# Performance work log

Hardware: AMD Instinct MI355X
Metric: run time of the kernel (lower is better)

## Reference

```python
import jax, jax.numpy as jnp
import numpy as np

T, B, H, C = 4096, 32, 512, 32000

def setup_inputs() -> dict:
    key = jax.random.key(0)
    k1, k2, k3, k4, k5 = jax.random.split(key, 5)
    decoder_output = jax.random.normal(k1, (T, B, H), dtype=jnp.float32)
    align_w = jax.random.normal(k2, (H,), dtype=jnp.float32) * (1.0 / np.sqrt(H))
    align_b = jax.random.normal(k3, (), dtype=jnp.float32) * 0.01
    out_w = jax.random.normal(k4, (C, H), dtype=jnp.float32) * (1.0 / np.sqrt(H))
    out_b = jax.random.normal(k5, (C,), dtype=jnp.float32) * 0.01
    return {"decoder_output": decoder_output, "align_w": align_w,
            "align_b": align_b, "out_w": out_w, "out_b": out_b}

def reference(decoder_output, align_w, align_b, out_w, out_b):
    # e[b,t] = tanh(align(decoder_output[t,b]))  -- vectorized over (t,b)
    e = jnp.tanh(jnp.einsum('tbh,h->bt', decoder_output, align_w) + align_b)  # [B,T]
    alpha = jax.nn.softmax(e, axis=-1)                                        # [B,T]
    context = jnp.einsum('bt,tbh->bh', alpha, decoder_output)                 # [B,H]
    return context @ out_w.T + out_b                                          # [B,C]
```

## Files before the change

### kernel.cpp

```cpp
#include <hip/hip_runtime.h>
#include <hip/hip_bf16.h>
#include <math.h>

#define TT 4096
#define BB 32
#define HH 512
#define CC 32000
#define NCHUNK 64
#define TPC 64
#define HQ 4
#define OSLICE (BB*CC)
#define OW_PAD 36

#define WS_CTX    0
#define WS_LPART  16384
#define WS_BIG    18432

__device__ __forceinline__ float dot4(const float4 a, const float4 b) {
  return fmaf(a.w, b.w, fmaf(a.z, b.z, fmaf(a.y, b.y, fmaf(a.x, b.x, 0.f))));
}

__global__ __launch_bounds__(256) void k1_partials(
    const float* __restrict__ dec, const float* __restrict__ aw,
    const float* __restrict__ abp,
    float* __restrict__ ctx_part, float* __restrict__ l_part)
{
  const int chunk = blockIdx.x;
  const int b     = blockIdx.y;
  const int tid   = threadIdx.x;
  const int wv = tid >> 6, ln = tid & 63;
  const float ab = abp[0];
  const float4 aw0 = *(const float4*)(aw + ln*4);
  const float4 aw1 = *(const float4*)(aw + 256 + ln*4);

  const size_t rowstep = (size_t)BB*HH;
  const float* base = dec + ((size_t)(chunk*TPC + wv*16)*BB + b)*HH + (size_t)ln*4;

  float4 c0 = make_float4(0.f,0.f,0.f,0.f), c1 = make_float4(0.f,0.f,0.f,0.f);
  float l = 0.f;

  for (int it = 0; it < 16; it += 2) {
    const float* p0 = base + (size_t)it*rowstep;
    const float* p1 = base + (size_t)(it+1)*rowstep;
    const float4 xa0 = *(const float4*)(p0);
    const float4 xa1 = *(const float4*)(p0 + 256);
    const float4 xb0 = *(const float4*)(p1);
    const float4 xb1 = *(const float4*)(p1 + 256);
    float da = dot4(xa0, aw0) + dot4(xa1, aw1);
    float db = dot4(xb0, aw0) + dot4(xb1, aw1);
    #pragma unroll
    for (int off = 32; off > 0; off >>= 1) {
      da += __shfl_xor(da, off);
      db += __shfl_xor(db, off);
    }
    const float exa = __expf(2.f*(da + ab));
    const float exb = __expf(2.f*(db + ab));
    const float tha = 1.f - 2.f*__builtin_amdgcn_rcpf(exa + 1.f);
    const float thb = 1.f - 2.f*__builtin_amdgcn_rcpf(exb + 1.f);
    const float wa = __expf(tha);
    const float wb = __expf(thb);
    l += wa + wb;
    c0.x = fmaf(wa, xa0.x, fmaf(wb, xb0.x, c0.x));
    c0.y = fmaf(wa, xa0.y, fmaf(wb, xb0.y, c0.y));
    c0.z = fmaf(wa, xa0.z, fmaf(wb, xb0.z, c0.z));
    c0.w = fmaf(wa, xa0.w, fmaf(wb, xb0.w, c0.w));
    c1.x = fmaf(wa, xa1.x, fmaf(wb, xb1.x, c1.x));
    c1.y = fmaf(wa, xa1.y, fmaf(wb, xb1.y, c1.y));
    c1.z = fmaf(wa, xa1.z, fmaf(wb, xb1.z, c1.z));
    c1.w = fmaf(wa, xa1.w, fmaf(wb, xb1.w, c1.w));
  }

  __shared__ float s_ctx[4][HH];
  __shared__ float s_l[4];
  *(float4*)&s_ctx[wv][ln*4]       = c0;
  *(float4*)&s_ctx[wv][256 + ln*4] = c1;
  if (ln == 0) s_l[wv] = l;
  __syncthreads();
  if (tid < 128) {
    const int h = tid * 4;
    float4 a = make_float4(0.f,0.f,0.f,0.f);
    #pragma unroll
    for (int w2 = 0; w2 < 4; ++w2) {
      const float4 v = *(const float4*)&s_ctx[w2][h];
      a.x += v.x; a.y += v.y; a.z += v.z; a.w += v.w;
    }
    const size_t pp = (size_t)b*NCHUNK + chunk;
    *(float4*)(ctx_part + pp*HH + h) = a;
    if (tid == 0) l_part[pp] = s_l[0] + s_l[1] + s_l[2] + s_l[3];
  }
}

__global__ __launch_bounds__(128) void k2_combine(
    const float* __restrict__ ctx_part, const float* __restrict__ l_part,
    float* __restrict__ ctx)
{
  const int b = blockIdx.x;
  const int h = threadIdx.x * 4;
  float L = 0.f;
  for (int p = 0; p < NCHUNK; ++p) L += l_part[b*NCHUNK + p];
  float4 a = make_float4(0.f,0.f,0.f,0.f);
  for (int p = 0; p < NCHUNK; ++p) {
    const float4 v = *(const float4*)(ctx_part + ((size_t)b*NCHUNK + p)*HH + h);
    a.x += v.x; a.y += v.y; a.z += v.z; a.w += v.w;
  }
  const float inv = 1.f / L;
  *(float4*)(ctx + b*HH + h) = make_float4(a.x*inv, a.y*inv, a.z*inv, a.w*inv);
}

__global__ __launch_bounds__(256) void k3_matmul(
    const float* __restrict__ ctx, const float* __restrict__ ow,
    float* __restrict__ out_part)
{
  __shared__ float s_ow[256*OW_PAD];
  __shared__ float s_cx[32*128];
  const int tid = threadIdx.x;
  const int ci = tid & 63, wv = tid >> 6;
  const int hq = blockIdx.x, cblk = blockIdx.y;
  const int h0 = hq * 128;
  const int crow0 = cblk * 256;

  #pragma unroll
  for (int rep = 0; rep < 4; ++rep) {
    const int j = rep*1024 + tid*4;
    const int b = j >> 7, hh = j & 127;
    *(float4*)&s_cx[j] = *(const float4*)(ctx + (size_t)b*HH + h0 + hh);
  }

  float acc[4][8];
  #pragma unroll
  for (int g = 0; g < 4; ++g)
    #pragma unroll
    for (int bi = 0; bi < 8; ++bi) acc[g][bi] = 0.f;

  for (int ch = 0; ch < 4; ++ch) {
    if (ch) __syncthreads();
    #pragma unroll
    for (int rep = 0; rep < 8; ++rep) {
      const int j = rep*256 + tid;
      const int r = j >> 3, hp = j & 7;
      *(float4*)&s_ow[r*OW_PAD + hp*4] =
          *(const float4*)(ow + (size_t)(crow0 + r)*HH + h0 + ch*32 + hp*4);
    }
    __syncthreads();
    #pragma unroll
    for (int s = 0; s < 8; ++s) {
      float4 w4[4];
      #pragma unroll
      for (int g = 0; g < 4; ++g)
        w4[g] = *(const float4*)&s_ow[(g*64 + ci)*OW_PAD + s*4];
      #pragma unroll
      for (int bi = 0; bi < 8; ++bi) {
        const float4 c4 = *(const float4*)&s_cx[(wv*8 + bi)*128 + ch*32 + s*4];
        #pragma unroll
        for (int g = 0; g < 4; ++g) {
          acc[g][bi] = fmaf(w4[g].w, c4.w, fmaf(w4[g].z, c4.z,
                       fmaf(w4[g].y, c4.y, fmaf(w4[g].x, c4.x, acc[g][bi]))));
        }
      }
    }
  }

  float* op = out_part + (size_t)hq*OSLICE;
  #pragma unroll
  for (int bi = 0; bi < 8; ++bi) {
    #pragma unroll
    for (int g = 0; g < 4; ++g)
      op[(size_t)(wv*8 + bi)*CC + crow0 + g*64 + ci] = acc[g][bi];
  }
}

__global__ __launch_bounds__(256) void k4_final(
    const float* __restrict__ out_part, const float* __restrict__ ob,
    float* __restrict__ out)
{
  const size_t i = ((size_t)blockIdx.x * 256 + threadIdx.x) * 4;
  float4 r = *(const float4*)(out_part + i);
  #pragma unroll
  for (int q = 1; q < HQ; ++q) {
    const float4 p = *(const float4*)(out_part + (size_t)q*OSLICE + i);
    r.x += p.x; r.y += p.y; r.z += p.z; r.w += p.w;
  }
  const int cIdx = (int)(i % CC);
  const float4 b4 = *(const float4*)(ob + cIdx);
  *(float4*)(out + i) = make_float4(r.x+b4.x, r.y+b4.y, r.z+b4.z, r.w+b4.w);
}

extern "C" void kernel_launch(void* const* d_in, const int* in_sizes, int n_in,
                              void* d_out, int out_size, void* d_ws, size_t ws_size,
                              hipStream_t stream) {
  const float* dec = (const float*)d_in[0];
  const float* aw  = (const float*)d_in[1];
  const float* ab  = (const float*)d_in[2];
  const float* ow  = (const float*)d_in[3];
  const float* ob  = (const float*)d_in[4];
  float* out = (float*)d_out;
  float* ws  = (float*)d_ws;
  float* ctx   = ws + WS_CTX;
  float* lpart = ws + WS_LPART;
  float* big   = ws + WS_BIG;

  k1_partials<<<dim3(NCHUNK, BB), 256, 0, stream>>>(dec, aw, ab, big, lpart);
  k2_combine<<<dim3(BB), 128, 0, stream>>>(big, lpart, ctx);
  k3_matmul<<<dim3(HQ, 125), 256, 0, stream>>>(ctx, ow, big);
  k4_final<<<dim3((BB*CC)/(256*4)), 256, 0, stream>>>(big, ob, out);
}
```

Measured before the change: 89.80 us.

## Drop split-K partials, fuse bias into matmul, double-buffer weight tiles

The output matmul now assigns each block 128 classes across the full hidden dimension rather than splitting H four ways. This removes the partial-output buffer round trip and the separate final reduction kernel, and the bias is added directly in the matmul epilogue. Weight tiles are double-buffered in shared memory with register prefetch, and the context combine kernel splits its chunk reduction across two thread halves. The cost is larger shared memory per block (the whole context) and a longer serial K loop per block, which may reduce occupancy.

```diff
diff --git a/kernel.cpp b/kernel.cpp
--- a/kernel.cpp
+++ b/kernel.cpp
@@ -8,8 +8,9 @@
 #define CC 32000
 #define NCHUNK 64
 #define TPC 64
-#define HQ 4
-#define OSLICE (BB*CC)
+#define K3_CPB 128
+#define K3_CH 32
+#define K3_NCH 16
 #define OW_PAD 36
 
 #define WS_CTX    0
@@ -90,99 +91,115 @@
   }
 }
 
-__global__ __launch_bounds__(128) void k2_combine(
+__global__ __launch_bounds__(256) void k2_combine(
     const float* __restrict__ ctx_part, const float* __restrict__ l_part,
     float* __restrict__ ctx)
 {
   const int b = blockIdx.x;
-  const int h = threadIdx.x * 4;
-  float L = 0.f;
-  for (int p = 0; p < NCHUNK; ++p) L += l_part[b*NCHUNK + p];
+  const int tid = threadIdx.x;
+  const int half = tid >> 7, hf = tid & 127;
+  const int h = hf * 4;
+
   float4 a = make_float4(0.f,0.f,0.f,0.f);
-  for (int p = 0; p < NCHUNK; ++p) {
-    const float4 v = *(const float4*)(ctx_part + ((size_t)b*NCHUNK + p)*HH + h);
+  const float* basep = ctx_part + ((size_t)b*NCHUNK + half*32)*HH + h;
+  #pragma unroll 8
+  for (int p = 0; p < 32; ++p) {
+    const float4 v = *(const float4*)(basep + (size_t)p*HH);
     a.x += v.x; a.y += v.y; a.z += v.z; a.w += v.w;
   }
-  const float inv = 1.f / L;
-  *(float4*)(ctx + b*HH + h) = make_float4(a.x*inv, a.y*inv, a.z*inv, a.w*inv);
+
+  __shared__ float4 s_part[2][128];
+  __shared__ float s_L;
+  s_part[half][hf] = a;
+  if (tid < 64) {
+    float Lv = l_part[b*NCHUNK + tid];
+    #pragma unroll
+    for (int off = 32; off > 0; off >>= 1) Lv += __shfl_xor(Lv, off);
+    if (tid == 0) s_L = Lv;
+  }
+  __syncthreads();
+  if (tid < 128) {
+    const float4 r0 = s_part[0][tid];
+    const float4 r1 = s_part[1][tid];
+    const float inv = 1.f / s_L;
+    *(float4*)(ctx + (size_t)b*HH + tid*4) = make_float4(
+        (r0.x+r1.x)*inv, (r0.y+r1.y)*inv, (r0.z+r1.z)*inv, (r0.w+r1.w)*inv);
+  }
 }
 
 __global__ __launch_bounds__(256) void k3_matmul(
     const float* __restrict__ ctx, const float* __restrict__ ow,
-    float* __restrict__ out_part)
+    const float* __restrict__ ob, float* __restrict__ out)
 {
-  __shared__ float s_ow[256*OW_PAD];
-  __shared__ float s_cx[32*128];
+  __shared__ float s_cx[BB*HH];
+  __shared__ float s_ow[2][K3_CPB*OW_PAD];
   const int tid = threadIdx.x;
   const int ci = tid & 63, wv = tid >> 6;
-  const int hq = blockIdx.x, cblk = blockIdx.y;
-  const int h0 = hq * 128;
-  const int crow0 = cblk * 256;
-
+  const int crow0 = blockIdx.x * K3_CPB;
+
+  #pragma unroll
+  for (int rep = 0; rep < 16; ++rep) {
+    const int j = rep*1024 + tid*4;
+    *(float4*)&s_cx[j] = *(const float4*)(ctx + j);
+  }
   #pragma unroll
   for (int rep = 0; rep < 4; ++rep) {
-    const int j = rep*1024 + tid*4;
-    const int b = j >> 7, hh = j & 127;
-    *(float4*)&s_cx[j] = *(const float4*)(ctx + (size_t)b*HH + h0 + hh);
-  }
-
-  float acc[4][8];
-  #pragma unroll
-  for (int g = 0; g < 4; ++g)
+    const int j = rep*256 + tid;
+    const int r = j >> 3, hp = j & 7;
+    *(float4*)&s_ow[0][r*OW_PAD + hp*4] =
+        *(const float4*)(ow + (size_t)(crow0 + r)*HH + hp*4);
+  }
+  __syncthreads();
+
+  float acc[2][8];
+  #pragma unroll
+  for (int g = 0; g < 2; ++g)
     #pragma unroll
     for (int bi = 0; bi < 8; ++bi) acc[g][bi] = 0.f;
 
-  for (int ch = 0; ch < 4; ++ch) {
-    if (ch) __syncthreads();
-    #pragma unroll
-    for (int rep = 0; rep < 8; ++rep) {
-      const int j = rep*256 + tid;
-      const int r = j >> 3, hp = j & 7;
-      *(float4*)&s_ow[r*OW_PAD + hp*4] =
-          *(const float4*)(ow + (size_t)(crow0 + r)*HH + h0 + ch*32 + hp*4);
-    }
-    __syncthreads();
+  for (int ch = 0; ch < K3_NCH; ++ch) {
+    const int buf = ch & 1;
+    float4 pre[4];
+    if (ch < K3_NCH-1) {
+      #pragma unroll
+      for (int rep = 0; rep < 4; ++rep) {
+        const int j = rep*256 + tid;
+        const int r = j >> 3, hp = j & 7;
+        pre[rep] = *(const float4*)(ow + (size_t)(crow0 + r)*HH + (ch+1)*K3_CH + hp*4);
+      }
+    }
     #pragma unroll
     for (int s = 0; s < 8; ++s) {
-      float4 w4[4];
-      #pragma unroll
-      for (int g = 0; g < 4; ++g)
-        w4[g] = *(const float4*)&s_ow[(g*64 + ci)*OW_PAD + s*4];
+      float4 w4[2];
+      w4[0] = *(const float4*)&s_ow[buf][(ci)*OW_PAD + s*4];
+      w4[1] = *(const float4*)&s_ow[buf][(64 + ci)*OW_PAD + s*4];
       #pragma unroll
       for (int bi = 0; bi < 8; ++bi) {
-        const float4 c4 = *(const float4*)&s_cx[(wv*8 + bi)*128 + ch*32 + s*4];
-        #pragma unroll
-        for (int g = 0; g < 4; ++g) {
-          acc[g][bi] = fmaf(w4[g].w, c4.w, fmaf(w4[g].z, c4.z,
-                       fmaf(w4[g].y, c4.y, fmaf(w4[g].x, c4.x, acc[g][bi]))));
-        }
+        const float4 c4 = *(const float4*)&s_cx[(wv*8 + bi)*HH + ch*K3_CH + s*4];
+        acc[0][bi] = fmaf(w4[0].w, c4.w, fmaf(w4[0].z, c4.z,
+                     fmaf(w4[0].y, c4.y, fmaf(w4[0].x, c4.x, acc[0][bi]))));
+        acc[1][bi] = fmaf(w4[1].w, c4.w, fmaf(w4[1].z, c4.z,
+                     fmaf(w4[1].y, c4.y, fmaf(w4[1].x, c4.x, acc[1][bi]))));
       }
     }
-  }
-
-  float* op = out_part + (size_t)hq*OSLICE;
+    if (ch < K3_NCH-1) {
+      #pragma unroll
+      for (int rep = 0; rep < 4; ++rep) {
+        const int j = rep*256 + tid;
+        const int r = j >> 3, hp = j & 7;
+        *(float4*)&s_ow[buf^1][r*OW_PAD + hp*4] = pre[rep];
+      }
+      __syncthreads();
+    }
+  }
+
+  const float bias0 = ob[crow0 + ci];
+  const float bias1 = ob[crow0 + 64 + ci];
   #pragma unroll
   for (int bi = 0; bi < 8; ++bi) {
-    #pragma unroll
-    for (int g = 0; g < 4; ++g)
-      op[(size_t)(wv*8 + bi)*CC + crow0 + g*64 + ci] = acc[g][bi];
-  }
-}
-
-__global__ __launch_bounds__(256) void k4_final(
-    const float* __restrict__ out_part, const float* __restrict__ ob,
-    float* __restrict__ out)
-{
-  const size_t i = ((size_t)blockIdx.x * 256 + threadIdx.x) * 4;
-  float4 r = *(const float4*)(out_part + i);
-  #pragma unroll
-  for (int q = 1; q < HQ; ++q) {
-    const float4 p = *(const float4*)(out_part + (size_t)q*OSLICE + i);
-    r.x += p.x; r.y += p.y; r.z += p.z; r.w += p.w;
-  }
-  const int cIdx = (int)(i % CC);
-  const float4 b4 = *(const float4*)(ob + cIdx);
-  *(float4*)(out + i) = make_float4(r.x+b4.x, r.y+b4.y, r.z+b4.z, r.w+b4.w);
+    out[(size_t)(wv*8 + bi)*CC + crow0 + ci]      = acc[0][bi] + bias0;
+    out[(size_t)(wv*8 + bi)*CC + crow0 + 64 + ci] = acc[1][bi] + bias1;
+  }
 }
 
 extern "C" void kernel_launch(void* const* d_in, const int* in_sizes, int n_in,
@@ -200,7 +217,6 @@
   float* big   = ws + WS_BIG;
 
   k1_partials<<<dim3(NCHUNK, BB), 256, 0, stream>>>(dec, aw, ab, big, lpart);
-  k2_combine<<<dim3(BB), 128, 0, stream>>>(big, lpart, ctx);
-  k3_matmul<<<dim3(HQ, 125), 256, 0, stream>>>(ctx, ow, big);
-  k4_final<<<dim3((BB*CC)/(256*4)), 256, 0, stream>>>(big, ob, out);
-}
+  k2_combine<<<dim3(BB), 256, 0, stream>>>(big, lpart, ctx);
+  k3_matmul<<<dim3(CC/K3_CPB), 256, 0, stream>>>(ctx, ow, ob, out);
+}
```

After: 128.4 us. 1.43x slower.
